# Performance work log

Measured on AMD Instinct MI355X. Metric: run time of the kernel, lower is better.

Reference implementation:

```python
import math
import jax, jax.numpy as jnp
import numpy as np

D = 256      # embedding_dim (= internal_dim, downsample_rate 1)
H = 8        # num_heads
HD = D // H  # head_dim = 32
NTC = 16     # num_text_classes
NIMG = 4096  # image tokens (64x64)
N = NIMG + NTC
B = 2
NKE = 64     # num_k_exclude_rope


def _rope(x, freqs):
    # x: (b, h, n, c); freqs: (n, c//2, 2) = (cos, sin) of complex rotary factors
    b, h, n, c = x.shape
    xp = x.reshape(b, h, n, c // 2, 2)
    cos, sin = freqs[..., 0], freqs[..., 1]
    xr, xi = xp[..., 0], xp[..., 1]
    out_r = xr * cos - xi * sin
    out_i = xr * sin + xi * cos
    return jnp.stack([out_r, out_i], axis=-1).reshape(b, h, n, c)


def _sep_heads(x):
    b, n, c = x.shape
    return x.reshape(b, n, H, c // H).transpose(0, 2, 1, 3)  # (b,h,n,hd)


def setup_inputs() -> dict:
    key = jax.random.key(0)
    ks = jax.random.split(key, 14)
    s = 0.02
    # rotary factors: unit-norm cos/sin pairs
    ang_img = jax.random.uniform(ks[3], (NIMG, HD // 2)) * (2.0 * np.pi)
    ang_txt = jax.random.uniform(ks[4], (NTC, HD // 2)) * (2.0 * np.pi)
    return {
        "q": jax.random.normal(ks[0], (B, N, D), dtype=jnp.float32),
        "k": jax.random.normal(ks[1], (B, N, D), dtype=jnp.float32),
        "v": jax.random.normal(ks[2], (B, N, D), dtype=jnp.float32),
        "freqs_cis_img": jnp.stack([jnp.cos(ang_img), jnp.sin(ang_img)], axis=-1),
        "freqs_cis_txt": jnp.stack([jnp.cos(ang_txt), jnp.sin(ang_txt)], axis=-1),
        "Wq": jax.random.normal(ks[5], (D, D), dtype=jnp.float32) * s,
        "bq": jnp.zeros((D,), dtype=jnp.float32),
        "Wk": jax.random.normal(ks[6], (D, D), dtype=jnp.float32) * s,
        "bk": jnp.zeros((D,), dtype=jnp.float32),
        "Wv": jax.random.normal(ks[7], (D, D), dtype=jnp.float32) * s,
        "bv": jnp.zeros((D,), dtype=jnp.float32),
        "Wo": jax.random.normal(ks[8], (D, D), dtype=jnp.float32) * s,
        "bo": jnp.zeros((D,), dtype=jnp.float32),
        "num_k_exclude_rope": NKE,
    }


def reference(q, k, v, freqs_cis_img, freqs_cis_txt,
              Wq, bq, Wk, bk, Wv, bv, Wo, bo, num_k_exclude_rope):
    q = q @ Wq.T + bq
    k = k @ Wk.T + bk
    v = v @ Wv.T + bv
    q = _sep_heads(q)  # (b,h,n,hd)
    k = _sep_heads(k)
    v = _sep_heads(v)

    # split tokens into image / text regions, apply RoPE separately
    q_img, q_txt = q[:, :, :-NTC, :], q[:, :, -NTC:, :]
    k_img, k_txt = k[:, :, :-NTC, :], k[:, :, -NTC:, :]
    q_img = _rope(q_img, freqs_cis_img)
    k_img = _rope(k_img, freqs_cis_img)
    q_txt = _rope(q_txt, freqs_cis_txt)
    k_txt = _rope(k_txt, freqs_cis_txt)
    q = jnp.concatenate([q_img, q_txt], axis=-2)
    k = jnp.concatenate([k_img, k_txt], axis=-2)

    scale = 1.0 / math.sqrt(HD)
    nke = num_k_exclude_rope
    if nke > 0:
        k_td, k_mem = k[:, :, :-nke, :], k[:, :, -nke:, :]
        v_td, v_mem = v[:, :, :-nke, :], v[:, :, -nke:, :]
        attn = jax.nn.softmax(jnp.einsum('bhqd,bhkd->bhqk', q, k_td) * scale, axis=-1)
        out = jnp.einsum('bhqk,bhkd->bhqd', attn, v_td)
        attn_m = jax.nn.softmax(jnp.einsum('bhqd,bhkd->bhqk', q, k_mem) * scale, axis=-1)
        out = out + jnp.einsum('bhqk,bhkd->bhqd', attn_m, v_mem)
    else:
        attn = jax.nn.softmax(jnp.einsum('bhqd,bhkd->bhqk', q, k) * scale, axis=-1)
        out = jnp.einsum('bhqk,bhkd->bhqd', attn, v)

    b, h, n, hd = out.shape
    out = out.transpose(0, 2, 1, 3).reshape(b, n, h * hd)
    return out @ Wo.T + bo
```

## Files before the change

### kernel.cpp

```cpp
#include <hip/hip_runtime.h>
#include <hip/hip_bf16.h>

#define BN    4112
#define NKR   4160
#define BNP   4160
#define BB    2
#define HH    8
#define NIMG_ 4096
#define NMAIN 4048
#define MROWS 8224
#define QSCALE 0.25505402f

typedef __attribute__((ext_vector_type(8))) short short8;
typedef __attribute__((ext_vector_type(4))) float f32x4;
typedef __attribute__((ext_vector_type(16))) float f32x16;

__device__ __forceinline__ unsigned short f2bs(float x) { return __bfloat16_as_ushort(__float2bfloat16(x)); }
__device__ __forceinline__ unsigned pkbf(float a, float b) {
    __hip_bfloat162 h = __float22bfloat162_rn(make_float2(a, b));
    unsigned u; __builtin_memcpy(&u, &h, 4); return u;
}
__device__ __forceinline__ float fexp2(float x) {
#if __has_builtin(__builtin_amdgcn_exp2f)
    return __builtin_amdgcn_exp2f(x);
#else
    return exp2f(x);
#endif
}

__global__ __launch_bounds__(256)
void prep_w(const float* __restrict__ Wq, const float* __restrict__ Wk,
            const float* __restrict__ Wv, const float* __restrict__ Wo,
            short* __restrict__ Wb)
{
    const int i   = blockIdx.x * 256 + threadIdx.x;
    const int m   = i >> 13;
    const int off = (i & 8191) * 8;
    const float* W = (m == 0) ? Wq : (m == 1) ? Wk : (m == 2) ? Wv : Wo;
    float4 a0 = *(const float4*)(W + off), a1 = *(const float4*)(W + off + 4);
    *(uint4*)(Wb + (size_t)m * 65536 + off) =
        uint4{pkbf(a0.x, a0.y), pkbf(a0.z, a0.w), pkbf(a1.x, a1.y), pkbf(a1.z, a1.w)};
}

__global__ __launch_bounds__(256)
void qkv_mfma(const float* __restrict__ Aq, const float* __restrict__ Ak, const float* __restrict__ Av,
              const short* __restrict__ Wb,
              const float* __restrict__ bq, const float* __restrict__ bk, const float* __restrict__ bv,
              short* __restrict__ Qr, short* __restrict__ Kr, short* __restrict__ Vt,
              const float* __restrict__ fimg, const float* __restrict__ ftxt)
{
    __shared__ __align__(16) short Ws[2][64][72];
    __shared__ __align__(16) short Ds[2][64][72];

    const int mode = blockIdx.z;
    const float* A    = (mode == 0) ? Aq : (mode == 1) ? Ak : Av;
    const float* bias = (mode == 0) ? bq : (mode == 1) ? bk : bv;

    const int t    = threadIdx.x;
    const int wave = t >> 6, lane = t & 63, q16 = lane & 15, quad = lane >> 4;
    const int f0 = blockIdx.x * 64;
    const int m0 = blockIdx.y * 64;
    const int sr = t >> 2, sc = (t & 3) * 16;
    const int arow = m0 + sr;
    const bool aval = arow < MROWS;
    const short* wp = Wb + (size_t)mode * 65536 + (size_t)(f0 + sr) * 256 + sc;
    const float* ap = A + (size_t)(aval ? arow : 0) * 256 + sc;

    f32x4 acc[4] = {{0,0,0,0},{0,0,0,0},{0,0,0,0},{0,0,0,0}};

    uint4 wr0, wr1, dr0, dr1;
    {
        wr0 = *(const uint4*)(wp); wr1 = *(const uint4*)(wp + 8);
        float4 a0 = *(const float4*)(ap);     float4 a1 = *(const float4*)(ap + 4);
        float4 a2 = *(const float4*)(ap + 8); float4 a3 = *(const float4*)(ap + 12);
        dr0 = uint4{pkbf(a0.x,a0.y), pkbf(a0.z,a0.w), pkbf(a1.x,a1.y), pkbf(a1.z,a1.w)};
        dr1 = uint4{pkbf(a2.x,a2.y), pkbf(a2.z,a2.w), pkbf(a3.x,a3.y), pkbf(a3.z,a3.w)};
    }
    *(uint4*)&Ws[0][sr][sc] = wr0; *(uint4*)&Ws[0][sr][sc + 8] = wr1;
    *(uint4*)&Ds[0][sr][sc] = dr0; *(uint4*)&Ds[0][sr][sc + 8] = dr1;
    __syncthreads();

    #pragma unroll
    for (int ki = 0; ki < 4; ++ki) {
        const int buf = ki & 1;
        if (ki < 3) {
            const int k1 = (ki + 1) * 64;
            wr0 = *(const uint4*)(wp + k1); wr1 = *(const uint4*)(wp + k1 + 8);
            float4 a0 = *(const float4*)(ap + k1);     float4 a1 = *(const float4*)(ap + k1 + 4);
            float4 a2 = *(const float4*)(ap + k1 + 8); float4 a3 = *(const float4*)(ap + k1 + 12);
            dr0 = uint4{pkbf(a0.x,a0.y), pkbf(a0.z,a0.w), pkbf(a1.x,a1.y), pkbf(a1.z,a1.w)};
            dr1 = uint4{pkbf(a2.x,a2.y), pkbf(a2.z,a2.w), pkbf(a3.x,a3.y), pkbf(a3.z,a3.w)};
        }
        #pragma unroll
        for (int ks = 0; ks < 2; ++ks) {
            const short8 af = *(const short8*)&Ws[buf][wave * 16 + q16][ks * 32 + quad * 8];
            #pragma unroll
            for (int ct = 0; ct < 4; ++ct) {
                const short8 bf = *(const short8*)&Ds[buf][ct * 16 + q16][ks * 32 + quad * 8];
                acc[ct] = __builtin_amdgcn_mfma_f32_16x16x32_bf16(af, bf, acc[ct], 0, 0, 0);
            }
        }
        if (ki < 3) {
            *(uint4*)&Ws[buf ^ 1][sr][sc] = wr0; *(uint4*)&Ws[buf ^ 1][sr][sc + 8] = wr1;
            *(uint4*)&Ds[buf ^ 1][sr][sc] = dr0; *(uint4*)&Ds[buf ^ 1][sr][sc + 8] = dr1;
            __syncthreads();
        }
    }

    const int fbase = f0 + wave * 16 + quad * 4;
    const float4 bb = *(const float4*)(bias + fbase);
    float vs[4][4];
    #pragma unroll
    for (int ct = 0; ct < 4; ++ct) {
        int n = m0 + ct * 16 + q16;
        float v0 = acc[ct][0] + bb.x, v1 = acc[ct][1] + bb.y;
        float v2 = acc[ct][2] + bb.z, v3 = acc[ct][3] + bb.w;
        int b  = (n >= BN) ? 1 : 0;
        int nb = n - b * BN;
        if (mode < 2) {
            int j0 = (fbase & 31) >> 1;
            const float* fr = (nb < NIMG_) ? (fimg + ((size_t)nb * 16 + j0) * 2)
                                           : (ftxt + ((size_t)(nb - NIMG_) * 16 + j0) * 2);
            float4 cs = *(const float4*)fr;
            float r0 = v0 * cs.x - v1 * cs.y, i0 = v0 * cs.y + v1 * cs.x;
            float r1 = v2 * cs.z - v3 * cs.w, i1 = v2 * cs.w + v3 * cs.z;
            v0 = r0; v1 = i0; v2 = r1; v3 = i1;
        }
        if (mode == 2) {
            vs[ct][0] = v0; vs[ct][1] = v1; vs[ct][2] = v2; vs[ct][3] = v3;
            continue;
        }
        if (n >= MROWS) continue;
        const int h = (fbase >> 5) & 7, hd = fbase & 31;
        if (mode == 0) {
            unsigned short* op = (unsigned short*)Qr + (((size_t)(b * HH + h) * BN + nb) * 32 + hd);
            *(uint2*)op = uint2{pkbf(v0 * QSCALE, v1 * QSCALE), pkbf(v2 * QSCALE, v3 * QSCALE)};
        } else {
            int nk = nb + ((nb >= NMAIN) ? 48 : 0);
            unsigned short* op = (unsigned short*)Kr + (((size_t)(b * HH + h) * NKR + nk) * 32 + hd);
            *(uint2*)op = uint2{pkbf(v0, v1), pkbf(v2, v3)};
        }
    }

    if (mode == 2) {
        short (*Tr)[72] = Ds[0];
        const int fl = wave * 16 + quad * 4;
        #pragma unroll
        for (int ct = 0; ct < 4; ++ct) {
            const int nl = ct * 16 + q16;
            Tr[fl + 0][nl] = (short)f2bs(vs[ct][0]);
            Tr[fl + 1][nl] = (short)f2bs(vs[ct][1]);
            Tr[fl + 2][nl] = (short)f2bs(vs[ct][2]);
            Tr[fl + 3][nl] = (short)f2bs(vs[ct][3]);
        }
        __syncthreads();
        const int h0 = (f0 >> 5) & 7;
        #pragma unroll
        for (int ii = 0; ii < 2; ++ii) {
            const int r  = ii * 32 + (t >> 3);
            const int c8 = (t & 7) * 8;
            const int ng = m0 + c8;
            if (ng < MROWS) {
                uint4 val = *(const uint4*)&Tr[r][c8];
                int b  = (ng >= BN) ? 1 : 0;
                int nb = ng - b * BN;
                int nk = nb + ((nb >= NMAIN) ? 48 : 0);
                int h  = h0 + (r >> 5), hd = r & 31;
                unsigned short* op = (unsigned short*)Vt + ((size_t)(b * HH + h) * 32 + hd) * BNP + nk;
                *(uint4*)op = val;
            }
        }
    }

    if (blockIdx.x == 0 && blockIdx.y < 16 && t < 192) {
        const int bh = blockIdx.y;
        if (mode == 1) {
            short* base = Kr + (size_t)bh * NKR * 32 + (size_t)NMAIN * 32;
            *(uint4*)(base + t * 8) = uint4{0u, 0u, 0u, 0u};
        } else if (mode == 2) {
            short* base = Vt + (size_t)bh * 32 * BNP + (size_t)(t / 6) * BNP + NMAIN + (t % 6) * 8;
            *(uint4*)base = uint4{0u, 0u, 0u, 0u};
        }
    }
}

__global__ __launch_bounds__(256, 4)
void attn_mfma(const short* __restrict__ Qr, const short* __restrict__ Kr,
               const short* __restrict__ Vt, unsigned short* __restrict__ AO)
{
    __shared__ __align__(16) short Ks[2][2][64][40];
    __shared__ __align__(16) short Vs[2][2][32][72];

    const int t    = threadIdx.x;
    const int wave = t >> 6, lane = t & 63, q32 = lane & 31, hi = lane >> 5;
    const int grp  = wave >> 1, w2 = wave & 1;

    const int b_   = blockIdx.x;
    const int idx  = b_ >> 3;
    const int bh   = ((b_ & 7) << 1) + (idx >= 65 ? 1 : 0);
    const int bx   = idx - (idx >= 65 ? 65 : 0);

    const int q  = bx * 64 + w2 * 32 + q32;
    const int qc = (q < BN) ? q : (BN - 1);
    const short* qp = Qr + ((size_t)bh * BN + qc) * 32 + hi * 8;
    const short8 qf0 = *(const short8*)(qp);
    const short8 qf1 = *(const short8*)(qp + 16);

    f32x16 oAx = {0,0,0,0,0,0,0,0,0,0,0,0,0,0,0,0};
    f32x16 oAy = {0,0,0,0,0,0,0,0,0,0,0,0,0,0,0,0};
    f32x16 oBx = {0,0,0,0,0,0,0,0,0,0,0,0,0,0,0,0};
    const f32x16 z16 = {0,0,0,0,0,0,0,0,0,0,0,0,0,0,0,0};
    float LA = 0.f, LB = 0.f;

    const int tg = t & 127;
    const int kr = tg >> 2, kc = tg & 3;
    const int vr = tg >> 3, vc = tg & 7;
    const short* kg = Kr + (size_t)bh * NKR * 32 + (size_t)grp * 65536 + (size_t)kr * 32 + kc * 8;
    const short* vg = Vt + (size_t)bh * 32 * BNP + (size_t)vr * BNP + grp * 2048
                         + (vc >> 1) * 16 + (vc & 1) * 4;
    const int ntiles = 32 + grp;

    auto tile = [&](int buf, f32x16& ox, f32x16& oy, float& L) {
        const short8 kf00 = *(const short8*)&Ks[grp][buf][q32][hi * 8];
        const short8 kf01 = *(const short8*)&Ks[grp][buf][q32][16 + hi * 8];
        const short8 kf10 = *(const short8*)&Ks[grp][buf][32 + q32][hi * 8];
        const short8 kf11 = *(const short8*)&Ks[grp][buf][32 + q32][16 + hi * 8];
        f32x16 s0 = __builtin_amdgcn_mfma_f32_32x32x16_bf16(kf00, qf0, z16, 0, 0, 0);
        f32x16 s1 = __builtin_amdgcn_mfma_f32_32x32x16_bf16(kf10, qf0, z16, 0, 0, 0);
        s0 = __builtin_amdgcn_mfma_f32_32x32x16_bf16(kf01, qf1, s0, 0, 0, 0);
        s1 = __builtin_amdgcn_mfma_f32_32x32x16_bf16(kf11, qf1, s1, 0, 0, 0);
        float p0[16], p1[16];
        #pragma unroll
        for (int r = 0; r < 16; ++r) p0[r] = fexp2(s0[r]);
        #pragma unroll
        for (int r = 0; r < 16; ++r) p1[r] = fexp2(s1[r]);
        float l0 = (((p0[0]+p0[1])+(p0[2]+p0[3])) + ((p0[4]+p0[5])+(p0[6]+p0[7])))
                 + (((p0[8]+p0[9])+(p0[10]+p0[11])) + ((p0[12]+p0[13])+(p0[14]+p0[15])));
        float l1 = (((p1[0]+p1[1])+(p1[2]+p1[3])) + ((p1[4]+p1[5])+(p1[6]+p1[7])))
                 + (((p1[8]+p1[9])+(p1[10]+p1[11])) + ((p1[12]+p1[13])+(p1[14]+p1[15])));
        #pragma unroll
        for (int m = 0; m < 2; ++m) {
            uint4 pbu = uint4{pkbf(p0[8*m+0], p0[8*m+1]), pkbf(p0[8*m+2], p0[8*m+3]),
                              pkbf(p0[8*m+4], p0[8*m+5]), pkbf(p0[8*m+6], p0[8*m+7])};
            short8 pb; __builtin_memcpy(&pb, &pbu, 16);
            const short8 vf = *(const short8*)&Vs[grp][buf][q32][m * 16 + hi * 8];
            ox = __builtin_amdgcn_mfma_f32_32x32x16_bf16(vf, pb, ox, 0, 0, 0);
        }
        #pragma unroll
        for (int m = 0; m < 2; ++m) {
            uint4 pbu = uint4{pkbf(p1[8*m+0], p1[8*m+1]), pkbf(p1[8*m+2], p1[8*m+3]),
                              pkbf(p1[8*m+4], p1[8*m+5]), pkbf(p1[8*m+6], p1[8*m+7])};
            short8 pb; __builtin_memcpy(&pb, &pbu, 16);
            const short8 vf = *(const short8*)&Vs[grp][buf][q32][32 + m * 16 + hi * 8];
            oy = __builtin_amdgcn_mfma_f32_32x32x16_bf16(vf, pb, oy, 0, 0, 0);
        }
        L += l0 + l1;
    };

    *(uint4*)&Ks[grp][0][kr][kc * 8]      = *(const uint4*)(kg);
    *(uint4*)&Ks[grp][0][kr + 32][kc * 8] = *(const uint4*)(kg + 1024);
    {
        uint2 a0 = *(const uint2*)(vg),              b0 = *(const uint2*)(vg + 8);
        uint2 a1 = *(const uint2*)(vg + 16 * BNP),   b1 = *(const uint2*)(vg + 16 * BNP + 8);
        *(uint4*)&Vs[grp][0][vr][vc * 8]      = uint4{a0.x, a0.y, b0.x, b0.y};
        *(uint4*)&Vs[grp][0][vr + 16][vc * 8] = uint4{a1.x, a1.y, b1.x, b1.y};
    }
    __syncthreads();

    for (int it = 0; it < 33; ++it) {
        const int buf = it & 1;
        uint4 kreg0, kreg1; uint2 va0, vb0, va1, vb1;
        const bool pre = (it + 1) < ntiles;
        if (pre) {
            const short* kp = kg + (size_t)(it + 1) * 2048;
            kreg0 = *(const uint4*)(kp);
            kreg1 = *(const uint4*)(kp + 1024);
            const short* vp = vg + (it + 1) * 64;
            va0 = *(const uint2*)(vp);            vb0 = *(const uint2*)(vp + 8);
            va1 = *(const uint2*)(vp + 16 * BNP); vb1 = *(const uint2*)(vp + 16 * BNP + 8);
        }
        if (it < ntiles) {
            __builtin_amdgcn_s_setprio(1);
            if (grp == 0 || it < 32) tile(buf, oAx, oAy, LA);
            else                     tile(buf, oBx, oBx, LB);
            __builtin_amdgcn_s_setprio(0);
        }
        if (pre) {
            *(uint4*)&Ks[grp][buf ^ 1][kr][kc * 8]      = kreg0;
            *(uint4*)&Ks[grp][buf ^ 1][kr + 32][kc * 8] = kreg1;
            *(uint4*)&Vs[grp][buf ^ 1][vr][vc * 8]      = uint4{va0.x, va0.y, vb0.x, vb0.y};
            *(uint4*)&Vs[grp][buf ^ 1][vr + 16][vc * 8] = uint4{va1.x, va1.y, vb1.x, vb1.y};
        }
        __syncthreads();
    }

    f32x16 oA = oAx + oAy;
    f32x16 oB = oBx;

    LA += __shfl_xor(LA, 32);
    LB += __shfl_xor(LB, 32);

    float* ex = (float*)&Ks[0][0][0][0];
    const int slot = (w2 * 64 + lane) * 20;
    if (grp == 0) {
        #pragma unroll
        for (int i = 0; i < 4; ++i)
            *(f32x4*)(ex + slot + 4 * i) = f32x4{oA[4*i], oA[4*i+1], oA[4*i+2], oA[4*i+3]};
        ex[slot + 16] = LA;
    }
    __syncthreads();

    if (grp == 1 && q < BN) {
        float LT = LA + ex[slot + 16] - 48.f;
        const float iA = 1.f / LT, iB = 1.f / LB;
        const int b = bh >> 3, h = bh & 7;
        unsigned short* ap = AO + ((size_t)b * BN + q) * 256 + h * 32;
        #pragma unroll
        for (int k = 0; k < 4; ++k) {
            f32x4 a = *(const f32x4*)(ex + slot + 4 * k);
            float w0 = (oA[4*k+0] + a[0]) * iA + oB[4*k+0] * iB;
            float w1 = (oA[4*k+1] + a[1]) * iA + oB[4*k+1] * iB;
            float w2 = (oA[4*k+2] + a[2]) * iA + oB[4*k+2] * iB;
            float w3 = (oA[4*k+3] + a[3]) * iA + oB[4*k+3] * iB;
            *(uint2*)(ap + 8 * k + 4 * hi) = uint2{pkbf(w0, w1), pkbf(w2, w3)};
        }
    }
}

__global__ __launch_bounds__(256)
void gemm_out(const unsigned short* __restrict__ A, const short* __restrict__ Wb,
              const float* __restrict__ bias, float* __restrict__ out)
{
    __shared__ __align__(16) short Ws[2][64][72];
    __shared__ __align__(16) short Ds[2][64][72];
    const int t    = threadIdx.x;
    const int wave = t >> 6, lane = t & 63, q16 = lane & 15, quad = lane >> 4;
    const int f0 = blockIdx.x * 64, m0 = blockIdx.y * 64;
    const int sr = t >> 2, sc = (t & 3) * 16;
    const int arow = m0 + sr;
    const bool aval = arow < MROWS;
    const short* wp = Wb + (size_t)3 * 65536 + (size_t)(f0 + sr) * 256 + sc;
    const unsigned short* ap = A + (size_t)(aval ? arow : 0) * 256 + sc;

    f32x4 acc[4] = {{0,0,0,0},{0,0,0,0},{0,0,0,0},{0,0,0,0}};

    uint4 wr0, wr1, dr0, dr1;
    {
        wr0 = *(const uint4*)(wp); wr1 = *(const uint4*)(wp + 8);
        dr0 = *(const uint4*)(ap); dr1 = *(const uint4*)(ap + 8);
    }
    *(uint4*)&Ws[0][sr][sc] = wr0; *(uint4*)&Ws[0][sr][sc + 8] = wr1;
    *(uint4*)&Ds[0][sr][sc] = dr0; *(uint4*)&Ds[0][sr][sc + 8] = dr1;
    __syncthreads();

    #pragma unroll
    for (int ki = 0; ki < 4; ++ki) {
        const int buf = ki & 1;
        if (ki < 3) {
            const int k1 = (ki + 1) * 64;
            wr0 = *(const uint4*)(wp + k1); wr1 = *(const uint4*)(wp + k1 + 8);
            dr0 = *(const uint4*)(ap + k1); dr1 = *(const uint4*)(ap + k1 + 8);
        }
        #pragma unroll
        for (int ks = 0; ks < 2; ++ks) {
            const short8 af = *(const short8*)&Ws[buf][wave * 16 + q16][ks * 32 + quad * 8];
            #pragma unroll
            for (int ct = 0; ct < 4; ++ct) {
                const short8 bf = *(const short8*)&Ds[buf][ct * 16 + q16][ks * 32 + quad * 8];
                acc[ct] = __builtin_amdgcn_mfma_f32_16x16x32_bf16(af, bf, acc[ct], 0, 0, 0);
            }
        }
        if (ki < 3) {
            *(uint4*)&Ws[buf ^ 1][sr][sc] = wr0; *(uint4*)&Ws[buf ^ 1][sr][sc + 8] = wr1;
            *(uint4*)&Ds[buf ^ 1][sr][sc] = dr0; *(uint4*)&Ds[buf ^ 1][sr][sc + 8] = dr1;
            __syncthreads();
        }
    }

    const int fbase = f0 + wave * 16 + quad * 4;
    const float4 bb = *(const float4*)(bias + fbase);
    #pragma unroll
    for (int ct = 0; ct < 4; ++ct) {
        int n = m0 + ct * 16 + q16;
        if (n >= MROWS) continue;
        float* op = out + (size_t)n * 256 + fbase;
        *(float4*)op = float4{acc[ct][0] + bb.x, acc[ct][1] + bb.y,
                              acc[ct][2] + bb.z, acc[ct][3] + bb.w};
    }
}

extern "C" void kernel_launch(void* const* d_in, const int* in_sizes, int n_in,
                              void* d_out, int out_size, void* d_ws, size_t ws_size,
                              hipStream_t stream)
{
    (void)in_sizes; (void)n_in; (void)out_size; (void)ws_size;
    const float* q    = (const float*)d_in[0];
    const float* k    = (const float*)d_in[1];
    const float* v    = (const float*)d_in[2];
    const float* fimg = (const float*)d_in[3];
    const float* ftxt = (const float*)d_in[4];
    const float* Wq   = (const float*)d_in[5];
    const float* bq   = (const float*)d_in[6];
    const float* Wk   = (const float*)d_in[7];
    const float* bk   = (const float*)d_in[8];
    const float* Wv   = (const float*)d_in[9];
    const float* bv   = (const float*)d_in[10];
    const float* Wo   = (const float*)d_in[11];
    const float* bo   = (const float*)d_in[12];

    char* w = (char*)d_ws;
    short*          Qr = (short*)(w);
    short*          Kr = (short*)(w + 4210688);
    short*          Vt = (short*)(w + 8470528);
    unsigned short* AO = (unsigned short*)(w + 12730368);
    short*          Wb = (short*)(w + 16941056);

    prep_w<<<dim3(128), 256, 0, stream>>>(Wq, Wk, Wv, Wo, Wb);
    qkv_mfma<<<dim3(4, 129, 3), 256, 0, stream>>>(q, k, v, Wb, bq, bk, bv,
                                                  Qr, Kr, Vt, fimg, ftxt);
    attn_mfma<<<dim3(1040), 256, 0, stream>>>(Qr, Kr, Vt, AO);
    gemm_out<<<dim3(4, 129), 256, 0, stream>>>(AO, Wb, bo, (float*)d_out);
}
```

Baseline: 192.6 us.

## Split attention keys across four wave groups and load V directly into registers

The attention block grows from 256 to 512 threads. The key range is split four ways (16 or 17 tiles per group) instead of two, so each wave runs about half as many loop iterations. V fragments are now read straight from global memory into registers rather than staged in shared memory, which removes the Vs buffer and its LDS traffic. The final reduction merges partial outputs from three groups through shared memory. In exchange, launch bounds of 512×8 tighten the register budget and add uncoalesced global loads for V.

```diff
diff --git a/kernel.cpp b/kernel.cpp
--- a/kernel.cpp
+++ b/kernel.cpp
@@ -184,43 +184,51 @@
     }
 }
 
-__global__ __launch_bounds__(256, 4)
+__global__ __launch_bounds__(512, 8)
 void attn_mfma(const short* __restrict__ Qr, const short* __restrict__ Kr,
                const short* __restrict__ Vt, unsigned short* __restrict__ AO)
 {
-    __shared__ __align__(16) short Ks[2][2][64][40];
-    __shared__ __align__(16) short Vs[2][2][32][72];
+    __shared__ __align__(16) short Ks[4][2][64][40];
 
     const int t    = threadIdx.x;
     const int wave = t >> 6, lane = t & 63, q32 = lane & 31, hi = lane >> 5;
-    const int grp  = wave >> 1, w2 = wave & 1;
+    const int grp  = wave & 3;
+    const int qg   = wave >> 2;
 
     const int b_   = blockIdx.x;
     const int idx  = b_ >> 3;
     const int bh   = ((b_ & 7) << 1) + (idx >= 65 ? 1 : 0);
     const int bx   = idx - (idx >= 65 ? 65 : 0);
 
-    const int q  = bx * 64 + w2 * 32 + q32;
+    const int q  = bx * 64 + qg * 32 + q32;
     const int qc = (q < BN) ? q : (BN - 1);
     const short* qp = Qr + ((size_t)bh * BN + qc) * 32 + hi * 8;
     const short8 qf0 = *(const short8*)(qp);
     const short8 qf1 = *(const short8*)(qp + 16);
 
-    f32x16 oAx = {0,0,0,0,0,0,0,0,0,0,0,0,0,0,0,0};
-    f32x16 oAy = {0,0,0,0,0,0,0,0,0,0,0,0,0,0,0,0};
-    f32x16 oBx = {0,0,0,0,0,0,0,0,0,0,0,0,0,0,0,0};
+    f32x16 oA = {0,0,0,0,0,0,0,0,0,0,0,0,0,0,0,0};
+    f32x16 oB = {0,0,0,0,0,0,0,0,0,0,0,0,0,0,0,0};
     const f32x16 z16 = {0,0,0,0,0,0,0,0,0,0,0,0,0,0,0,0};
     float LA = 0.f, LB = 0.f;
 
-    const int tg = t & 127;
-    const int kr = tg >> 2, kc = tg & 3;
-    const int vr = tg >> 3, vc = tg & 7;
-    const short* kg = Kr + (size_t)bh * NKR * 32 + (size_t)grp * 65536 + (size_t)kr * 32 + kc * 8;
-    const short* vg = Vt + (size_t)bh * 32 * BNP + (size_t)vr * BNP + grp * 2048
-                         + (vc >> 1) * 16 + (vc & 1) * 4;
-    const int ntiles = 32 + grp;
-
-    auto tile = [&](int buf, f32x16& ox, f32x16& oy, float& L) {
+    const int tg2 = qg * 64 + lane;
+    const int kr = tg2 >> 2, kc = tg2 & 3;
+    const short* kg = Kr + (size_t)bh * NKR * 32 + (size_t)grp * 32768
+                         + (size_t)kr * 32 + kc * 8;
+    const short* vbase = Vt + (size_t)bh * 32 * BNP + (size_t)q32 * BNP
+                            + grp * 1024 + hi * 4;
+    const int ntw = (grp == 3) ? 17 : 16;
+
+    uint2 v0a, v0b, v1a, v1b, v2a, v2b, v3a, v3b;
+    auto vload = [&](int it2) {
+        const short* vp = vbase + it2 * 64;
+        v0a = *(const uint2*)(vp);      v0b = *(const uint2*)(vp + 8);
+        v1a = *(const uint2*)(vp + 16); v1b = *(const uint2*)(vp + 24);
+        v2a = *(const uint2*)(vp + 32); v2b = *(const uint2*)(vp + 40);
+        v3a = *(const uint2*)(vp + 48); v3b = *(const uint2*)(vp + 56);
+    };
+
+    auto tile = [&](int buf, f32x16& o, float& L) {
         const short8 kf00 = *(const short8*)&Ks[grp][buf][q32][hi * 8];
         const short8 kf01 = *(const short8*)&Ks[grp][buf][q32][16 + hi * 8];
         const short8 kf10 = *(const short8*)&Ks[grp][buf][32 + q32][hi * 8];
@@ -238,90 +246,101 @@
                  + (((p0[8]+p0[9])+(p0[10]+p0[11])) + ((p0[12]+p0[13])+(p0[14]+p0[15])));
         float l1 = (((p1[0]+p1[1])+(p1[2]+p1[3])) + ((p1[4]+p1[5])+(p1[6]+p1[7])))
                  + (((p1[8]+p1[9])+(p1[10]+p1[11])) + ((p1[12]+p1[13])+(p1[14]+p1[15])));
-        #pragma unroll
-        for (int m = 0; m < 2; ++m) {
-            uint4 pbu = uint4{pkbf(p0[8*m+0], p0[8*m+1]), pkbf(p0[8*m+2], p0[8*m+3]),
-                              pkbf(p0[8*m+4], p0[8*m+5]), pkbf(p0[8*m+6], p0[8*m+7])};
+        {
+            uint4 pbu = uint4{pkbf(p0[0], p0[1]), pkbf(p0[2], p0[3]),
+                              pkbf(p0[4], p0[5]), pkbf(p0[6], p0[7])};
             short8 pb; __builtin_memcpy(&pb, &pbu, 16);
-            const short8 vf = *(const short8*)&Vs[grp][buf][q32][m * 16 + hi * 8];
-            ox = __builtin_amdgcn_mfma_f32_32x32x16_bf16(vf, pb, ox, 0, 0, 0);
-        }
-        #pragma unroll
-        for (int m = 0; m < 2; ++m) {
-            uint4 pbu = uint4{pkbf(p1[8*m+0], p1[8*m+1]), pkbf(p1[8*m+2], p1[8*m+3]),
-                              pkbf(p1[8*m+4], p1[8*m+5]), pkbf(p1[8*m+6], p1[8*m+7])};
+            uint4 vfu = uint4{v0a.x, v0a.y, v0b.x, v0b.y};
+            short8 vf; __builtin_memcpy(&vf, &vfu, 16);
+            o = __builtin_amdgcn_mfma_f32_32x32x16_bf16(vf, pb, o, 0, 0, 0);
+        }
+        {
+            uint4 pbu = uint4{pkbf(p0[8], p0[9]),  pkbf(p0[10], p0[11]),
+                              pkbf(p0[12], p0[13]), pkbf(p0[14], p0[15])};
             short8 pb; __builtin_memcpy(&pb, &pbu, 16);
-            const short8 vf = *(const short8*)&Vs[grp][buf][q32][32 + m * 16 + hi * 8];
-            oy = __builtin_amdgcn_mfma_f32_32x32x16_bf16(vf, pb, oy, 0, 0, 0);
+            uint4 vfu = uint4{v1a.x, v1a.y, v1b.x, v1b.y};
+            short8 vf; __builtin_memcpy(&vf, &vfu, 16);
+            o = __builtin_amdgcn_mfma_f32_32x32x16_bf16(vf, pb, o, 0, 0, 0);
+        }
+        {
+            uint4 pbu = uint4{pkbf(p1[0], p1[1]), pkbf(p1[2], p1[3]),
+                              pkbf(p1[4], p1[5]), pkbf(p1[6], p1[7])};
+            short8 pb; __builtin_memcpy(&pb, &pbu, 16);
+            uint4 vfu = uint4{v2a.x, v2a.y, v2b.x, v2b.y};
+            short8 vf; __builtin_memcpy(&vf, &vfu, 16);
+            o = __builtin_amdgcn_mfma_f32_32x32x16_bf16(vf, pb, o, 0, 0, 0);
+        }
+        {
+            uint4 pbu = uint4{pkbf(p1[8], p1[9]),  pkbf(p1[10], p1[11]),
+                              pkbf(p1[12], p1[13]), pkbf(p1[14], p1[15])};
+            short8 pb; __builtin_memcpy(&pb, &pbu, 16);
+            uint4 vfu = uint4{v3a.x, v3a.y, v3b.x, v3b.y};
+            short8 vf; __builtin_memcpy(&vf, &vfu, 16);
+            o = __builtin_amdgcn_mfma_f32_32x32x16_bf16(vf, pb, o, 0, 0, 0);
         }
         L += l0 + l1;
     };
 
     *(uint4*)&Ks[grp][0][kr][kc * 8]      = *(const uint4*)(kg);
     *(uint4*)&Ks[grp][0][kr + 32][kc * 8] = *(const uint4*)(kg + 1024);
-    {
-        uint2 a0 = *(const uint2*)(vg),              b0 = *(const uint2*)(vg + 8);
-        uint2 a1 = *(const uint2*)(vg + 16 * BNP),   b1 = *(const uint2*)(vg + 16 * BNP + 8);
-        *(uint4*)&Vs[grp][0][vr][vc * 8]      = uint4{a0.x, a0.y, b0.x, b0.y};
-        *(uint4*)&Vs[grp][0][vr + 16][vc * 8] = uint4{a1.x, a1.y, b1.x, b1.y};
-    }
+    vload(0);
     __syncthreads();
 
-    for (int it = 0; it < 33; ++it) {
+    for (int it = 0; it < 17; ++it) {
         const int buf = it & 1;
-        uint4 kreg0, kreg1; uint2 va0, vb0, va1, vb1;
-        const bool pre = (it + 1) < ntiles;
+        uint4 kreg0, kreg1;
+        const bool pre = (it + 1) < ntw;
         if (pre) {
             const short* kp = kg + (size_t)(it + 1) * 2048;
             kreg0 = *(const uint4*)(kp);
             kreg1 = *(const uint4*)(kp + 1024);
-            const short* vp = vg + (it + 1) * 64;
-            va0 = *(const uint2*)(vp);            vb0 = *(const uint2*)(vp + 8);
-            va1 = *(const uint2*)(vp + 16 * BNP); vb1 = *(const uint2*)(vp + 16 * BNP + 8);
-        }
-        if (it < ntiles) {
+        }
+        if (it < ntw) {
             __builtin_amdgcn_s_setprio(1);
-            if (grp == 0 || it < 32) tile(buf, oAx, oAy, LA);
-            else                     tile(buf, oBx, oBx, LB);
+            if (grp == 3 && it == 16) tile(buf, oB, LB);
+            else                      tile(buf, oA, LA);
             __builtin_amdgcn_s_setprio(0);
         }
         if (pre) {
+            vload(it + 1);
             *(uint4*)&Ks[grp][buf ^ 1][kr][kc * 8]      = kreg0;
             *(uint4*)&Ks[grp][buf ^ 1][kr + 32][kc * 8] = kreg1;
-            *(uint4*)&Vs[grp][buf ^ 1][vr][vc * 8]      = uint4{va0.x, va0.y, vb0.x, vb0.y};
-            *(uint4*)&Vs[grp][buf ^ 1][vr + 16][vc * 8] = uint4{va1.x, va1.y, vb1.x, vb1.y};
         }
         __syncthreads();
     }
-
-    f32x16 oA = oAx + oAy;
-    f32x16 oB = oBx;
 
     LA += __shfl_xor(LA, 32);
     LB += __shfl_xor(LB, 32);
 
-    float* ex = (float*)&Ks[0][0][0][0];
-    const int slot = (w2 * 64 + lane) * 20;
-    if (grp == 0) {
+    float* exO = (float*)&Ks[0][0][0][0];
+    float* exL = exO + 6 * 64 * 16;
+    if (grp < 3) {
+        const int sidx = (qg * 3 + grp) * 64 + lane;
+        float* po = exO + sidx * 16;
         #pragma unroll
         for (int i = 0; i < 4; ++i)
-            *(f32x4*)(ex + slot + 4 * i) = f32x4{oA[4*i], oA[4*i+1], oA[4*i+2], oA[4*i+3]};
-        ex[slot + 16] = LA;
+            *(f32x4*)(po + 4 * i) = f32x4{oA[4*i], oA[4*i+1], oA[4*i+2], oA[4*i+3]};
+        exL[sidx] = LA;
     }
     __syncthreads();
 
-    if (grp == 1 && q < BN) {
-        float LT = LA + ex[slot + 16] - 48.f;
+    if (grp == 3 && q < BN) {
+        const int s0i = (qg * 3 + 0) * 64 + lane;
+        const int s1i = (qg * 3 + 1) * 64 + lane;
+        const int s2i = (qg * 3 + 2) * 64 + lane;
+        float LT = LA + exL[s0i] + exL[s1i] + exL[s2i] - 48.f;
         const float iA = 1.f / LT, iB = 1.f / LB;
         const int b = bh >> 3, h = bh & 7;
         unsigned short* ap = AO + ((size_t)b * BN + q) * 256 + h * 32;
         #pragma unroll
         for (int k = 0; k < 4; ++k) {
-            f32x4 a = *(const f32x4*)(ex + slot + 4 * k);
-            float w0 = (oA[4*k+0] + a[0]) * iA + oB[4*k+0] * iB;
-            float w1 = (oA[4*k+1] + a[1]) * iA + oB[4*k+1] * iB;
-            float w2 = (oA[4*k+2] + a[2]) * iA + oB[4*k+2] * iB;
-            float w3 = (oA[4*k+3] + a[3]) * iA + oB[4*k+3] * iB;
+            f32x4 a0 = *(const f32x4*)(exO + s0i * 16 + 4 * k);
+            f32x4 a1 = *(const f32x4*)(exO + s1i * 16 + 4 * k);
+            f32x4 a2 = *(const f32x4*)(exO + s2i * 16 + 4 * k);
+            float w0 = (oA[4*k+0] + a0[0] + a1[0] + a2[0]) * iA + oB[4*k+0] * iB;
+            float w1 = (oA[4*k+1] + a0[1] + a1[1] + a2[1]) * iA + oB[4*k+1] * iB;
+            float w2 = (oA[4*k+2] + a0[2] + a1[2] + a2[2]) * iA + oB[4*k+2] * iB;
+            float w3 = (oA[4*k+3] + a0[3] + a1[3] + a2[3]) * iA + oB[4*k+3] * iB;
             *(uint2*)(ap + 8 * k + 4 * hi) = uint2{pkbf(w0, w1), pkbf(w2, w3)};
         }
     }
@@ -418,6 +437,6 @@
     prep_w<<<dim3(128), 256, 0, stream>>>(Wq, Wk, Wv, Wo, Wb);
     qkv_mfma<<<dim3(4, 129, 3), 256, 0, stream>>>(q, k, v, Wb, bq, bk, bv,
                                                   Qr, Kr, Vt, fimg, ftxt);
-    attn_mfma<<<dim3(1040), 256, 0, stream>>>(Qr, Kr, Vt, AO);
+    attn_mfma<<<dim3(1040), 512, 0, stream>>>(Qr, Kr, Vt, AO);
     gemm_out<<<dim3(4, 129), 256, 0, stream>>>(AO, Wb, bo, (float*)d_out);
 }
```

Result: slower. 523.8 us (+171.9%).
